# Kernel tuning notes

Measured on AMD Instinct MI355X. Metric: run time of the kernel, lower is better.

Reference implementation:

```python
import jax, jax.numpy as jnp
import numpy as np

N = 30000      # nodes
E = 480000     # edges (before self loops)
DIN = 128      # dim_in
DH = 32        # dim_h (per-head out channels)
H1 = 8         # gat1 heads
H2 = 2         # gat2 heads
G = 64         # num graphs in batch
DOUT = 10      # dim_out
NEG_SLOPE = 0.2


def _glorot(key, shape):
    fan_in = shape[0]
    return jax.random.normal(key, shape, dtype=jnp.float32) / np.sqrt(fan_in)


def setup_inputs() -> dict:
    key = jax.random.key(0)
    ks = jax.random.split(key, 16)
    x = jax.random.normal(ks[0], (N, DIN), dtype=jnp.float32)
    edge_index = jax.random.randint(ks[1], (2, E), 0, N, dtype=jnp.int32)
    batch = jnp.sort(jax.random.randint(ks[2], (N,), 0, G, dtype=jnp.int32))
    # GATv2Conv layer 1: lin_l, lin_r (dim_in -> H1*DH), att (H1, DH), bias (H1*DH)
    W1l = _glorot(ks[3], (DIN, H1 * DH))
    W1r = _glorot(ks[4], (DIN, H1 * DH))
    a1 = _glorot(ks[5], (DH, H1)).T  # [H1, DH]
    b1 = jnp.zeros((H1 * DH,), dtype=jnp.float32)
    # GATv2Conv layer 2: (H1*DH -> H2*DH)
    W2l = _glorot(ks[6], (H1 * DH, H2 * DH))
    W2r = _glorot(ks[7], (H1 * DH, H2 * DH))
    a2 = _glorot(ks[8], (DH, H2)).T  # [H2, DH]
    b2 = jnp.zeros((H2 * DH,), dtype=jnp.float32)
    # MLP head: fc1(2*DH -> DH), fc2(DH -> DH//2), fc(DH//2 -> DOUT); stored [in,out]
    fc1_w = _glorot(ks[9], (2 * DH, DH)); fc1_b = jnp.zeros((DH,), jnp.float32)
    fc2_w = _glorot(ks[10], (DH, DH // 2)); fc2_b = jnp.zeros((DH // 2,), jnp.float32)
    fc_w = _glorot(ks[11], (DH // 2, DOUT)); fc_b = jnp.zeros((DOUT,), jnp.float32)
    return {"x": x, "edge_index": edge_index, "batch": batch,
            "W1l": W1l, "W1r": W1r, "a1": a1, "b1": b1,
            "W2l": W2l, "W2r": W2r, "a2": a2, "b2": b2,
            "fc1_w": fc1_w, "fc1_b": fc1_b, "fc2_w": fc2_w, "fc2_b": fc2_b,
            "fc_w": fc_w, "fc_b": fc_b}


def gatv2_conv(x, edge_index, Wl, Wr, att, bias, heads, dh, n):
    """PyG GATv2Conv: concat=True, add_self_loops=True, negative_slope=0.2."""
    src, dst = edge_index[0], edge_index[1]
    loop = jnp.arange(n, dtype=src.dtype)        # self loops (PyG default)
    src = jnp.concatenate([src, loop])
    dst = jnp.concatenate([dst, loop])
    xl = (x @ Wl).reshape(n, heads, dh)          # source transform
    xr = (x @ Wr).reshape(n, heads, dh)          # destination transform
    xj = xl[src]                                  # [Etot, H, dh] message features
    s = jax.nn.leaky_relu(xj + xr[dst], NEG_SLOPE)
    e = jnp.einsum('ehd,hd->eh', s, att)          # per-edge per-head score
    # segment softmax over incoming edges of each destination node
    m = jax.ops.segment_max(e, dst, num_segments=n)
    p = jnp.exp(e - m[dst])
    z = jax.ops.segment_sum(p, dst, num_segments=n)
    alpha = p / z[dst]                            # [Etot, H]
    out = jax.ops.segment_sum(xj * alpha[..., None], dst, num_segments=n)
    return out.reshape(n, heads * dh) + bias


def reference(x, edge_index, batch, W1l, W1r, a1, b1, W2l, W2r, a2, b2,
              fc1_w, fc1_b, fc2_w, fc2_b, fc_w, fc_b):
    h = gatv2_conv(x, edge_index, W1l, W1r, a1, b1, H1, DH, N)
    h = jax.nn.elu(h)
    h = gatv2_conv(h, edge_index, W2l, W2r, a2, b2, H2, DH, N)  # [N, 2*DH]
    # global_mean_pool
    sums = jax.ops.segment_sum(h, batch, num_segments=G)
    cnt = jax.ops.segment_sum(jnp.ones((N,), h.dtype), batch, num_segments=G)
    hg = sums / jnp.maximum(cnt, 1.0)[:, None]    # [G, 2*DH]
    x1 = jax.nn.relu(hg @ fc1_w + fc1_b)
    # dropout p=0.2 is identity in eval mode
    x2 = jax.nn.relu(x1 @ fc2_w + fc2_b)
    c = x2 @ fc_w + fc_b
    return (c, x2)
```

## Files before the change

### kernel.cpp

```cpp
#include <hip/hip_runtime.h>
#include <math.h>

#define DIN 128
#define DH  32
#define H1  8
#define H2  2
#define GNUM 64
#define DOUT 10
#define NEG_SLOPE 0.2f
#define SCAN_B 512

typedef __attribute__((ext_vector_type(8))) short sv8;
typedef __attribute__((ext_vector_type(4))) short sv4;
typedef __attribute__((ext_vector_type(4))) float fv4;

static __device__ __forceinline__ unsigned short f2bf(float f) {
    unsigned int u = __float_as_uint(f);
    unsigned int r = (u + 0x7fffu + ((u >> 16) & 1u)) >> 16;
    return (unsigned short)r;
}
static __device__ __forceinline__ float bf2f(unsigned short h) {
    return __uint_as_float(((unsigned int)h) << 16);
}

__global__ void k_prep(const float* __restrict__ W1l, const float* __restrict__ W1r,
                       const float* __restrict__ W2l, const float* __restrict__ W2r,
                       short* __restrict__ B1th, short* __restrict__ B1tl,
                       short* __restrict__ B2th, short* __restrict__ B2tl,
                       int* __restrict__ zbase, int nz) {
    int id = blockIdx.x * blockDim.x + threadIdx.x;
    if (id < nz) zbase[id] = 0;
    const int T1 = 512 * 128;
    const int T2 = 128 * 256;
    if (id < T1) {
        int n = id / 128, k = id - n * 128;
        float v = (n < 256) ? W1l[(size_t)k * 256 + n] : W1r[(size_t)k * 256 + (n - 256)];
        unsigned short h = f2bf(v);
        B1th[id] = (short)h;
        B1tl[id] = (short)f2bf(v - bf2f(h));
    } else if (id < T1 + T2) {
        int id2 = id - T1;
        int n = id2 / 256, k = id2 - n * 256;
        float v = (n < 64) ? W2l[(size_t)k * 64 + n] : W2r[(size_t)k * 64 + (n - 64)];
        unsigned short h = f2bf(v);
        B2th[id2] = (short)h;
        B2tl[id2] = (short)f2bf(v - bf2f(h));
    }
}

__global__ void k_deg(const int* __restrict__ dst, int* __restrict__ deg, int E, int n) {
    int i = blockIdx.x * blockDim.x + threadIdx.x;
    if (i < E) {
        atomicAdd(&deg[dst[i]], 1);
    } else if (i < E + n) {
        atomicAdd(&deg[i - E], 1);
    }
}

__global__ __launch_bounds__(SCAN_B)
void k_scan_partial(const int* __restrict__ deg, int* __restrict__ bsum, int n) {
    int i = blockIdx.x * SCAN_B + threadIdx.x;
    int v = (i < n) ? deg[i] : 0;
    #pragma unroll
    for (int m = 32; m >= 1; m >>= 1) v += __shfl_xor(v, m);
    __shared__ int red[SCAN_B / 64];
    if ((threadIdx.x & 63) == 0) red[threadIdx.x >> 6] = v;
    __syncthreads();
    if (threadIdx.x == 0) {
        int s = 0;
        #pragma unroll
        for (int k = 0; k < SCAN_B / 64; ++k) s += red[k];
        bsum[blockIdx.x] = s;
    }
}

__global__ __launch_bounds__(SCAN_B)
void k_scan_apply(int* __restrict__ deg, int* __restrict__ cursor,
                  const int* __restrict__ bsum, int n, int nb) {
    __shared__ int buf[SCAN_B];
    __shared__ int pfx_s, tot_s;
    const int t = threadIdx.x, b = blockIdx.x;
    if (t < 64) {
        int v = (t < nb) ? bsum[t] : 0;
        int incl = v;
        #pragma unroll
        for (int o = 1; o < 64; o <<= 1) {
            int w = __shfl_up(incl, o);
            if (t >= o) incl += w;
        }
        int pfx = (b == 0) ? 0 : __shfl(incl, b - 1);
        int tot = __shfl(incl, nb - 1);
        if (t == 0) { pfx_s = pfx; tot_s = tot; }
    }
    int i = b * SCAN_B + t;
    int v = (i < n) ? deg[i] : 0;
    buf[t] = v;
    __syncthreads();
    for (int o = 1; o < SCAN_B; o <<= 1) {
        int a = (t >= o) ? buf[t - o] : 0;
        __syncthreads();
        buf[t] += a;
        __syncthreads();
    }
    int excl = buf[t] - v + pfx_s;
    if (i < n) { deg[i] = excl; cursor[i] = excl; }
    if (b == 0 && t == 0) deg[n] = tot_s;
}

__global__ void k_scatter(const int* __restrict__ src, const int* __restrict__ dst,
                          int* __restrict__ cursor, int* __restrict__ csr_src, int E, int n) {
    int i = blockIdx.x * blockDim.x + threadIdx.x;
    if (i < E) {
        int d = dst[i];
        int pos = atomicAdd(&cursor[d], 1);
        csr_src[pos] = src[i];
    } else if (i < E + n) {
        int v = i - E;
        int pos = atomicAdd(&cursor[v], 1);
        csr_src[pos] = v;
    }
}

__global__ __launch_bounds__(256)
void k_gemm1(const float* __restrict__ A,
             const short* __restrict__ Bth, const short* __restrict__ Btl,
             unsigned short* __restrict__ C,
             int M, int K, int Ntot) {
    __shared__ union {
        struct { short hi[128 * 40]; short lo[128 * 40]; } a;
        float c[64 * 68];
    } sm;
    const int tid = threadIdx.x;
    const int lane = tid & 63;
    const int wid = tid >> 6;
    const int wm = wid & 1, wn = wid >> 1;
    const int m0 = blockIdx.x * 128;
    const int n0 = blockIdx.y * 128;
    const int l15 = lane & 15, q = lane >> 4;

    fv4 acc[4][4] = {};

    for (int kk = 0; kk < K; kk += 32) {
        __syncthreads();
        #pragma unroll
        for (int i = 0; i < 4; ++i) {
            int idx = tid + i * 256;
            int row = idx >> 3;
            int qq  = idx & 7;
            int mg  = m0 + row;
            float4 v = make_float4(0.f, 0.f, 0.f, 0.f);
            if (mg < M) v = *(const float4*)(A + (size_t)mg * K + kk + qq * 4);
            unsigned short hx = f2bf(v.x), hy = f2bf(v.y), hz = f2bf(v.z), hw = f2bf(v.w);
            sv4 hi = { (short)hx, (short)hy, (short)hz, (short)hw };
            sv4 lo = { (short)f2bf(v.x - bf2f(hx)), (short)f2bf(v.y - bf2f(hy)),
                       (short)f2bf(v.z - bf2f(hz)), (short)f2bf(v.w - bf2f(hw)) };
            *(sv4*)&sm.a.hi[row * 40 + qq * 4] = hi;
            *(sv4*)&sm.a.lo[row * 40 + qq * 4] = lo;
        }
        __syncthreads();

        sv8 bh[4], bl[4];
        #pragma unroll
        for (int fn = 0; fn < 4; ++fn) {
            int ng = n0 + wn * 64 + fn * 16 + l15;
            bh[fn] = *(const sv8*)(Bth + (size_t)ng * K + kk + q * 8);
            bl[fn] = *(const sv8*)(Btl + (size_t)ng * K + kk + q * 8);
        }
        #pragma unroll
        for (int fm = 0; fm < 4; ++fm) {
            int rl = wm * 64 + fm * 16 + l15;
            sv8 ah = *(const sv8*)&sm.a.hi[rl * 40 + q * 8];
            sv8 al = *(const sv8*)&sm.a.lo[rl * 40 + q * 8];
            #pragma unroll
            for (int fn = 0; fn < 4; ++fn) {
                acc[fm][fn] = __builtin_amdgcn_mfma_f32_16x16x32_bf16(ah, bh[fn], acc[fm][fn], 0, 0, 0);
                acc[fm][fn] = __builtin_amdgcn_mfma_f32_16x16x32_bf16(ah, bl[fn], acc[fm][fn], 0, 0, 0);
                acc[fm][fn] = __builtin_amdgcn_mfma_f32_16x16x32_bf16(al, bh[fn], acc[fm][fn], 0, 0, 0);
            }
        }
    }

    #pragma unroll
    for (int s = 0; s < 2; ++s) {
        #pragma unroll
        for (int cn = 0; cn < 2; ++cn) {
            __syncthreads();
            if (wm == s && wn == cn) {
                #pragma unroll
                for (int fm = 0; fm < 4; ++fm)
                    #pragma unroll
                    for (int fn = 0; fn < 4; ++fn)
                        #pragma unroll
                        for (int r = 0; r < 4; ++r)
                            sm.c[(fm * 16 + q * 4 + r) * 68 + fn * 16 + l15] = acc[fm][fn][r];
            }
            __syncthreads();
            int lr = tid >> 2;
            int grow = m0 + s * 64 + lr;
            if (grow < M) {
                #pragma unroll
                for (int k4 = 0; k4 < 4; ++k4) {
                    int jj = (tid & 3) + k4 * 4;
                    float4 vv = *(float4*)&sm.c[lr * 68 + jj * 4];
                    int gcol = n0 + cn * 64 + jj * 4;
                    ushort4 uu;
                    uu.x = f2bf(vv.x); uu.y = f2bf(vv.y);
                    uu.z = f2bf(vv.z); uu.w = f2bf(vv.w);
                    *(ushort4*)(C + (size_t)grow * Ntot + gcol) = uu;
                }
            }
        }
    }
}

__global__ __launch_bounds__(256)
void k_gemm_bf(const unsigned short* __restrict__ A, const short* __restrict__ Bth,
               const short* __restrict__ Btl,
               unsigned short* __restrict__ C,
               int M, int K, int Ntot) {
    __shared__ union {
        short a[128 * 40];
        float c[64 * 68];
    } sm;
    const int tid = threadIdx.x;
    const int lane = tid & 63;
    const int wid = tid >> 6;
    const int wm = wid & 1, wn = wid >> 1;
    const int m0 = blockIdx.x * 128;
    const int n0 = blockIdx.y * 128;
    const int l15 = lane & 15, q = lane >> 4;

    fv4 acc[4][4] = {};

    for (int kk = 0; kk < K; kk += 32) {
        __syncthreads();
        #pragma unroll
        for (int i = 0; i < 2; ++i) {
            int idx = tid + i * 256;
            int row = idx >> 2, qq = idx & 3;
            int mg = m0 + row;
            sv8 v = { 0, 0, 0, 0, 0, 0, 0, 0 };
            if (mg < M) v = *(const sv8*)(A + (size_t)mg * K + kk + qq * 8);
            *(sv8*)&sm.a[row * 40 + qq * 8] = v;
        }
        __syncthreads();

        sv8 bh[4], bl[4];
        #pragma unroll
        for (int fn = 0; fn < 4; ++fn) {
            int ng = n0 + wn * 64 + fn * 16 + l15;
            bh[fn] = *(const sv8*)(Bth + (size_t)ng * K + kk + q * 8);
            bl[fn] = *(const sv8*)(Btl + (size_t)ng * K + kk + q * 8);
        }
        #pragma unroll
        for (int fm = 0; fm < 4; ++fm) {
            int rl = wm * 64 + fm * 16 + l15;
            sv8 ah = *(const sv8*)&sm.a[rl * 40 + q * 8];
            #pragma unroll
            for (int fn = 0; fn < 4; ++fn) {
                acc[fm][fn] = __builtin_amdgcn_mfma_f32_16x16x32_bf16(ah, bh[fn], acc[fm][fn], 0, 0, 0);
                acc[fm][fn] = __builtin_amdgcn_mfma_f32_16x16x32_bf16(ah, bl[fn], acc[fm][fn], 0, 0, 0);
            }
        }
    }

    #pragma unroll
    for (int s = 0; s < 2; ++s) {
        #pragma unroll
        for (int cn = 0; cn < 2; ++cn) {
            __syncthreads();
            if (wm == s && wn == cn) {
                #pragma unroll
                for (int fm = 0; fm < 4; ++fm)
                    #pragma unroll
                    for (int fn = 0; fn < 4; ++fn)
                        #pragma unroll
                        for (int r = 0; r < 4; ++r)
                            sm.c[(fm * 16 + q * 4 + r) * 68 + fn * 16 + l15] = acc[fm][fn][r];
            }
            __syncthreads();
            int lr = tid >> 2;
            int grow = m0 + s * 64 + lr;
            if (grow < M) {
                #pragma unroll
                for (int k4 = 0; k4 < 4; ++k4) {
                    int jj = (tid & 3) + k4 * 4;
                    float4 vv = *(float4*)&sm.c[lr * 68 + jj * 4];
                    int gcol = n0 + cn * 64 + jj * 4;
                    ushort4 uu;
                    uu.x = f2bf(vv.x); uu.y = f2bf(vv.y);
                    uu.z = f2bf(vv.z); uu.w = f2bf(vv.w);
                    *(ushort4*)(C + (size_t)grow * Ntot + gcol) = uu;
                }
            }
        }
    }
}

__global__ __launch_bounds__(64)
void k_edge1(const unsigned short* __restrict__ XLR,
             const int* __restrict__ offs, const int* __restrict__ csr,
             const float* __restrict__ att, const float* __restrict__ bias,
             unsigned short* __restrict__ out, int n) {
    const int lane = threadIdx.x;
    const int v = blockIdx.x;
    const int li = lane & 31;
    const int half = lane >> 5;
    const uint4* XL4 = (const uint4*)XLR;
    float av[8], xr[8];
    #pragma unroll
    for (int k = 0; k < 8; ++k) av[k] = att[li * 8 + k];
    {
        uint4 u = XL4[(size_t)v * 64 + 32 + li];
        xr[0] = __uint_as_float(u.x << 16);  xr[1] = __uint_as_float(u.x & 0xffff0000u);
        xr[2] = __uint_as_float(u.y << 16);  xr[3] = __uint_as_float(u.y & 0xffff0000u);
        xr[4] = __uint_as_float(u.z << 16);  xr[5] = __uint_as_float(u.z & 0xffff0000u);
        xr[6] = __uint_as_float(u.w << 16);  xr[7] = __uint_as_float(u.w & 0xffff0000u);
    }
    float z = 0.f;
    float acc[8] = {};
    const int e0 = offs[v], e1 = offs[v + 1];
    for (int j0 = e0; j0 < e1; j0 += 4) {
        #pragma unroll
        for (int p = 0; p < 2; ++p) {
            int j = j0 + p * 2 + half;
            bool valid = (j < e1);
            int jj = valid ? j : (e1 - 1);
            int src = csr[jj];
            uint4 u = XL4[(size_t)src * 64 + li];
            float f[8];
            f[0] = __uint_as_float(u.x << 16);  f[1] = __uint_as_float(u.x & 0xffff0000u);
            f[2] = __uint_as_float(u.y << 16);  f[3] = __uint_as_float(u.y & 0xffff0000u);
            f[4] = __uint_as_float(u.z << 16);  f[5] = __uint_as_float(u.z & 0xffff0000u);
            f[6] = __uint_as_float(u.w << 16);  f[7] = __uint_as_float(u.w & 0xffff0000u);
            float s1 = 0.f, s2 = 0.f;
            #pragma unroll
            for (int k = 0; k < 8; ++k) {
                float t = f[k] + xr[k];
                s1 = fmaf(t, av[k], s1);
                s2 = fmaf(fabsf(t), av[k], s2);
            }
            float s = fmaf(0.6f, s1, 0.4f * s2);
            s += __shfl_xor(s, 1);
            s += __shfl_xor(s, 2);
            float w = valid ? __expf(s) : 0.f;
            z += w;
            #pragma unroll
            for (int k = 0; k < 8; ++k) acc[k] = fmaf(w, f[k], acc[k]);
        }
    }
    z += __shfl_xor(z, 32);
    #pragma unroll
    for (int k = 0; k < 8; ++k) acc[k] += __shfl_xor(acc[k], 32);
    if (half == 0) {
        const float rz = 1.f / z;
        unsigned int o[4];
        #pragma unroll
        for (int k2 = 0; k2 < 4; ++k2) {
            float lo = fmaf(acc[k2 * 2 + 0], rz, bias[li * 8 + k2 * 2 + 0]);
            float hi = fmaf(acc[k2 * 2 + 1], rz, bias[li * 8 + k2 * 2 + 1]);
            lo = (lo > 0.f) ? lo : (__expf(lo) - 1.f);
            hi = (hi > 0.f) ? hi : (__expf(hi) - 1.f);
            o[k2] = (unsigned int)f2bf(lo) | ((unsigned int)f2bf(hi) << 16);
        }
        uint4 ov = { o[0], o[1], o[2], o[3] };
        *(uint4*)(out + (size_t)v * 256 + li * 8) = ov;
    }
}

__global__ __launch_bounds__(64)
void k_edge2(const unsigned short* __restrict__ XLR,
             const int* __restrict__ offs, const int* __restrict__ csr,
             const float* __restrict__ att, const float* __restrict__ bias,
             float* __restrict__ out, int n) {
    const int lane = threadIdx.x;
    const int v = blockIdx.x;
    const int li = lane & 7;
    const int slot = lane >> 3;
    const uint4* XL4 = (const uint4*)XLR;
    float av[8], xr[8];
    #pragma unroll
    for (int k = 0; k < 8; ++k) av[k] = att[li * 8 + k];
    {
        uint4 u = XL4[(size_t)v * 16 + 8 + li];
        xr[0] = __uint_as_float(u.x << 16);  xr[1] = __uint_as_float(u.x & 0xffff0000u);
        xr[2] = __uint_as_float(u.y << 16);  xr[3] = __uint_as_float(u.y & 0xffff0000u);
        xr[4] = __uint_as_float(u.z << 16);  xr[5] = __uint_as_float(u.z & 0xffff0000u);
        xr[6] = __uint_as_float(u.w << 16);  xr[7] = __uint_as_float(u.w & 0xffff0000u);
    }
    float z = 0.f;
    float acc[8] = {};
    const int e0 = offs[v], e1 = offs[v + 1];
    for (int j0 = e0; j0 < e1; j0 += 8) {
        int j = j0 + slot;
        bool valid = (j < e1);
        int jj = valid ? j : (e1 - 1);
        int src = csr[jj];
        uint4 u = XL4[(size_t)src * 16 + li];
        float f[8];
        f[0] = __uint_as_float(u.x << 16);  f[1] = __uint_as_float(u.x & 0xffff0000u);
        f[2] = __uint_as_float(u.y << 16);  f[3] = __uint_as_float(u.y & 0xffff0000u);
        f[4] = __uint_as_float(u.z << 16);  f[5] = __uint_as_float(u.z & 0xffff0000u);
        f[6] = __uint_as_float(u.w << 16);  f[7] = __uint_as_float(u.w & 0xffff0000u);
        float s1 = 0.f, s2 = 0.f;
        #pragma unroll
        for (int k = 0; k < 8; ++k) {
            float t = f[k] + xr[k];
            s1 = fmaf(t, av[k], s1);
            s2 = fmaf(fabsf(t), av[k], s2);
        }
        float s = fmaf(0.6f, s1, 0.4f * s2);
        s += __shfl_xor(s, 1);
        s += __shfl_xor(s, 2);
        float w = valid ? __expf(s) : 0.f;
        z += w;
        #pragma unroll
        for (int k = 0; k < 8; ++k) acc[k] = fmaf(w, f[k], acc[k]);
    }
    z += __shfl_xor(z, 8);  z += __shfl_xor(z, 16);  z += __shfl_xor(z, 32);
    #pragma unroll
    for (int k = 0; k < 8; ++k) {
        acc[k] += __shfl_xor(acc[k], 8);
        acc[k] += __shfl_xor(acc[k], 16);
        acc[k] += __shfl_xor(acc[k], 32);
    }
    if (slot == 0) {
        const float rz = 1.f / z;
        float o[8];
        #pragma unroll
        for (int k = 0; k < 8; ++k)
            o[k] = fmaf(acc[k], rz, bias[li * 8 + k]);
        float4 o0 = { o[0], o[1], o[2], o[3] };
        float4 o1 = { o[4], o[5], o[6], o[7] };
        *(float4*)(out + (size_t)v * 64 + li * 8 + 0) = o0;
        *(float4*)(out + (size_t)v * 64 + li * 8 + 4) = o1;
    }
}

__global__ __launch_bounds__(256)
void k_pool_mlp(const float* __restrict__ out2, const int* __restrict__ batch,
                const float* __restrict__ fc1w, const float* __restrict__ fc1b,
                const float* __restrict__ fc2w, const float* __restrict__ fc2b,
                const float* __restrict__ fcw,  const float* __restrict__ fcb,
                float* __restrict__ outc, float* __restrict__ outx2, int n) {
    const int g = blockIdx.x;
    const int t = threadIdx.x;
    const int lane = t & 63;
    const int w = t >> 6;
    __shared__ float red[4][64];
    __shared__ float hg_s[64];
    __shared__ float x1_s[32];
    __shared__ float x2_s[16];

    int lo = 0, hi = n;
    while (lo < hi) { int mid = (lo + hi) >> 1; if (batch[mid] < g) lo = mid + 1; else hi = mid; }
    const int start = lo;
    hi = n;
    while (lo < hi) { int mid = (lo + hi) >> 1; if (batch[mid] < g + 1) lo = mid + 1; else hi = mid; }
    const int end = lo;

    float s = 0.f;
    for (int v = start + w; v < end; v += 4)
        s += out2[(size_t)v * 64 + lane];
    red[w][lane] = s;
    __syncthreads();
    if (w == 0) {
        float tot = red[0][lane] + red[1][lane] + red[2][lane] + red[3][lane];
        float cnt = fmaxf((float)(end - start), 1.0f);
        hg_s[lane] = tot / cnt;
    }
    __syncthreads();
    if (t < 32) {
        float a = fc1b[t];
        #pragma unroll
        for (int k = 0; k < 64; ++k) a = fmaf(hg_s[k], fc1w[k * 32 + t], a);
        x1_s[t] = fmaxf(a, 0.f);
    }
    __syncthreads();
    if (t < 16) {
        float a = fc2b[t];
        #pragma unroll
        for (int k = 0; k < 32; ++k) a = fmaf(x1_s[k], fc2w[k * 16 + t], a);
        x2_s[t] = fmaxf(a, 0.f);
    }
    __syncthreads();
    if (t < DOUT) {
        float a = fcb[t];
        #pragma unroll
        for (int k = 0; k < 16; ++k) a = fmaf(x2_s[k], fcw[k * 10 + t], a);
        outc[g * DOUT + t] = a;
    }
    if (t < 16) outx2[g * 16 + t] = x2_s[t];
}

extern "C" void kernel_launch(void* const* d_in, const int* in_sizes, int n_in,
                              void* d_out, int out_size, void* d_ws, size_t ws_size,
                              hipStream_t stream) {
    const float* x    = (const float*)d_in[0];
    const int*   ei   = (const int*)d_in[1];
    const int*   batch= (const int*)d_in[2];
    const float* W1l  = (const float*)d_in[3];
    const float* W1r  = (const float*)d_in[4];
    const float* a1   = (const float*)d_in[5];
    const float* b1   = (const float*)d_in[6];
    const float* W2l  = (const float*)d_in[7];
    const float* W2r  = (const float*)d_in[8];
    const float* a2   = (const float*)d_in[9];
    const float* b2   = (const float*)d_in[10];
    const float* fc1w = (const float*)d_in[11];
    const float* fc1b = (const float*)d_in[12];
    const float* fc2w = (const float*)d_in[13];
    const float* fc2b = (const float*)d_in[14];
    const float* fcw  = (const float*)d_in[15];
    const float* fcb  = (const float*)d_in[16];

    const int N = in_sizes[2];
    const int E = in_sizes[1] / 2;
    const int ET = E + N;
    const int* esrc = ei;
    const int* edst = ei + E;
    const int NB = (N + SCAN_B - 1) / SCAN_B;

    char* ws = (char*)d_ws;
    size_t off = 0;
    unsigned short* xlr1b = (unsigned short*)(ws + off); off += (size_t)N * 512 * 2;
    unsigned short* h1b  = (unsigned short*)(ws + off);  off += (size_t)N * 256 * 2;
    float* out2 = (float*)(ws + off);            off += (size_t)N * 64 * 4;
    int*   deg   = (int*)(ws + off);             off += ((size_t)(N + 1) * 4 + 255) & ~255ull;
    int*   cursor= (int*)(ws + off);             off += ((size_t)N * 4 + 255) & ~255ull;
    int*   csr   = (int*)(ws + off);             off += ((size_t)ET * 4 + 255) & ~255ull;
    int*   bsum  = (int*)(ws + off);             off += ((size_t)(NB + 1) * 4 + 255) & ~255ull;
    short* B1th  = (short*)(ws + off);           off += (size_t)512 * 128 * 2;
    short* B1tl  = (short*)(ws + off);           off += (size_t)512 * 128 * 2;
    short* B2th  = (short*)(ws + off);           off += (size_t)128 * 256 * 2;
    short* B2tl  = (short*)(ws + off);           off += (size_t)128 * 256 * 2;
    unsigned short* xlr2b = xlr1b;
    (void)ws_size; (void)n_in; (void)out_size;

    float* outc  = (float*)d_out;
    float* outx2 = (float*)d_out + GNUM * DOUT;

    const int prep_tot = 512 * 128 + 128 * 256;
    k_prep<<<(prep_tot + 255) / 256, 256, 0, stream>>>(
        W1l, W1r, W2l, W2r, B1th, B1tl, B2th, B2tl, deg, N + 1);

    int tb = 256;
    int gb = (ET + tb - 1) / tb;
    k_deg<<<gb, tb, 0, stream>>>(edst, deg, E, N);
    k_scan_partial<<<NB, SCAN_B, 0, stream>>>(deg, bsum, N);
    k_scan_apply<<<NB, SCAN_B, 0, stream>>>(deg, cursor, bsum, N, NB);
    k_scatter<<<gb, tb, 0, stream>>>(esrc, edst, cursor, csr, E, N);

    dim3 g1((N + 127) / 128, 4);
    k_gemm1<<<g1, 256, 0, stream>>>(x, B1th, B1tl, xlr1b, N, DIN, 512);

    k_edge1<<<N, 64, 0, stream>>>(xlr1b, deg, csr, a1, b1, h1b, N);

    dim3 g2((N + 127) / 128, 1);
    k_gemm_bf<<<g2, 256, 0, stream>>>(h1b, B2th, B2tl, xlr2b, N, 256, 128);

    k_edge2<<<N, 64, 0, stream>>>(xlr2b, deg, csr, a2, b2, out2, N);

    k_pool_mlp<<<GNUM, 256, 0, stream>>>(out2, batch, fc1w, fc1b, fc2w, fc2b,
                                         fcw, fcb, outc, outx2, N);
}
```

Baseline: 293.0 us.

## Pre-split x into bf16 hi/lo once and load GEMM operands directly from global

The fp32 input x is now converted to packed bf16 hi/lo rows in the prep kernel, so gemm1 no longer redoes the split for every column block. Both GEMMs drop the shared-memory A staging and its per-iteration barriers, loading MFMA fragments straight from global memory and relying on cache. gemm_bf is split into two column blocks of 64 for more parallelism, and launch bounds request two blocks per CU. In exchange there is an extra global buffer of N x 256 bf16 written and read, and the direct global fragment loads are less coalesced.

```diff
diff --git a/kernel.cpp b/kernel.cpp
--- a/kernel.cpp
+++ b/kernel.cpp
@@ -23,25 +23,39 @@
     return __uint_as_float(((unsigned int)h) << 16);
 }
 
-__global__ void k_prep(const float* __restrict__ W1l, const float* __restrict__ W1r,
+__global__ void k_prep(const float* __restrict__ x,
+                       const float* __restrict__ W1l, const float* __restrict__ W1r,
                        const float* __restrict__ W2l, const float* __restrict__ W2r,
+                       unsigned short* __restrict__ xg,
                        short* __restrict__ B1th, short* __restrict__ B1tl,
                        short* __restrict__ B2th, short* __restrict__ B2tl,
-                       int* __restrict__ zbase, int nz) {
+                       int* __restrict__ zbase, int nz, int n) {
     int id = blockIdx.x * blockDim.x + threadIdx.x;
     if (id < nz) zbase[id] = 0;
+    const int NX = n * 32;
     const int T1 = 512 * 128;
     const int T2 = 128 * 256;
-    if (id < T1) {
-        int n = id / 128, k = id - n * 128;
-        float v = (n < 256) ? W1l[(size_t)k * 256 + n] : W1r[(size_t)k * 256 + (n - 256)];
+    if (id < NX) {
+        int m = id >> 5, j = id & 31;
+        float4 v = *(const float4*)(x + (size_t)m * 128 + j * 4);
+        unsigned short hx = f2bf(v.x), hy = f2bf(v.y), hz = f2bf(v.z), hw = f2bf(v.w);
+        ushort4 hi; hi.x = hx; hi.y = hy; hi.z = hz; hi.w = hw;
+        ushort4 lo;
+        lo.x = f2bf(v.x - bf2f(hx)); lo.y = f2bf(v.y - bf2f(hy));
+        lo.z = f2bf(v.z - bf2f(hz)); lo.w = f2bf(v.w - bf2f(hw));
+        *(ushort4*)(xg + (size_t)m * 256 + j * 4) = hi;
+        *(ushort4*)(xg + (size_t)m * 256 + 128 + j * 4) = lo;
+    } else if (id < NX + T1) {
+        int id1 = id - NX;
+        int nn = id1 / 128, k = id1 - nn * 128;
+        float v = (nn < 256) ? W1l[(size_t)k * 256 + nn] : W1r[(size_t)k * 256 + (nn - 256)];
         unsigned short h = f2bf(v);
-        B1th[id] = (short)h;
-        B1tl[id] = (short)f2bf(v - bf2f(h));
-    } else if (id < T1 + T2) {
-        int id2 = id - T1;
-        int n = id2 / 256, k = id2 - n * 256;
-        float v = (n < 64) ? W2l[(size_t)k * 64 + n] : W2r[(size_t)k * 64 + (n - 64)];
+        B1th[id1] = (short)h;
+        B1tl[id1] = (short)f2bf(v - bf2f(h));
+    } else if (id < NX + T1 + T2) {
+        int id2 = id - NX - T1;
+        int nn = id2 / 256, k = id2 - nn * 256;
+        float v = (nn < 64) ? W2l[(size_t)k * 64 + nn] : W2r[(size_t)k * 64 + (nn - 64)];
         unsigned short h = f2bf(v);
         B2th[id2] = (short)h;
         B2tl[id2] = (short)f2bf(v - bf2f(h));
@@ -121,15 +135,12 @@
     }
 }
 
-__global__ __launch_bounds__(256)
-void k_gemm1(const float* __restrict__ A,
+__global__ __launch_bounds__(256, 2)
+void k_gemm1(const unsigned short* __restrict__ Ag,
              const short* __restrict__ Bth, const short* __restrict__ Btl,
              unsigned short* __restrict__ C,
-             int M, int K, int Ntot) {
-    __shared__ union {
-        struct { short hi[128 * 40]; short lo[128 * 40]; } a;
-        float c[64 * 68];
-    } sm;
+             int M, int Ntot) {
+    __shared__ float smc[64 * 68];
     const int tid = threadIdx.x;
     const int lane = tid & 63;
     const int wid = tid >> 6;
@@ -140,42 +151,43 @@
 
     fv4 acc[4][4] = {};
 
-    for (int kk = 0; kk < K; kk += 32) {
-        __syncthreads();
-        #pragma unroll
-        for (int i = 0; i < 4; ++i) {
-            int idx = tid + i * 256;
-            int row = idx >> 3;
-            int qq  = idx & 7;
-            int mg  = m0 + row;
-            float4 v = make_float4(0.f, 0.f, 0.f, 0.f);
-            if (mg < M) v = *(const float4*)(A + (size_t)mg * K + kk + qq * 4);
-            unsigned short hx = f2bf(v.x), hy = f2bf(v.y), hz = f2bf(v.z), hw = f2bf(v.w);
-            sv4 hi = { (short)hx, (short)hy, (short)hz, (short)hw };
-            sv4 lo = { (short)f2bf(v.x - bf2f(hx)), (short)f2bf(v.y - bf2f(hy)),
-                       (short)f2bf(v.z - bf2f(hz)), (short)f2bf(v.w - bf2f(hw)) };
-            *(sv4*)&sm.a.hi[row * 40 + qq * 4] = hi;
-            *(sv4*)&sm.a.lo[row * 40 + qq * 4] = lo;
-        }
-        __syncthreads();
-
-        sv8 bh[4], bl[4];
+    const unsigned short* arow[4];
+    #pragma unroll
+    for (int fm = 0; fm < 4; ++fm) {
+        int mg = m0 + wm * 64 + fm * 16 + l15;
+        if (mg >= M) mg = M - 1;
+        arow[fm] = Ag + (size_t)mg * 256;
+    }
+    const short* browh[4];
+    const short* browl[4];
+    #pragma unroll
+    for (int fn = 0; fn < 4; ++fn) {
+        int ng = n0 + wn * 64 + fn * 16 + l15;
+        browh[fn] = Bth + (size_t)ng * 128;
+        browl[fn] = Btl + (size_t)ng * 128;
+    }
+
+    #pragma unroll
+    for (int c = 0; c < 4; ++c) {
+        const int ko = c * 32 + q * 8;
+        sv8 ah[4], al[4], bh[4], bl[4];
         #pragma unroll
         for (int fn = 0; fn < 4; ++fn) {
-            int ng = n0 + wn * 64 + fn * 16 + l15;
-            bh[fn] = *(const sv8*)(Bth + (size_t)ng * K + kk + q * 8);
-            bl[fn] = *(const sv8*)(Btl + (size_t)ng * K + kk + q * 8);
+            bh[fn] = *(const sv8*)(browh[fn] + ko);
+            bl[fn] = *(const sv8*)(browl[fn] + ko);
         }
         #pragma unroll
         for (int fm = 0; fm < 4; ++fm) {
-            int rl = wm * 64 + fm * 16 + l15;
-            sv8 ah = *(const sv8*)&sm.a.hi[rl * 40 + q * 8];
-            sv8 al = *(const sv8*)&sm.a.lo[rl * 40 + q * 8];
+            ah[fm] = *(const sv8*)(arow[fm] + ko);
+            al[fm] = *(const sv8*)(arow[fm] + 128 + ko);
+        }
+        #pragma unroll
+        for (int fm = 0; fm < 4; ++fm) {
             #pragma unroll
             for (int fn = 0; fn < 4; ++fn) {
-                acc[fm][fn] = __builtin_amdgcn_mfma_f32_16x16x32_bf16(ah, bh[fn], acc[fm][fn], 0, 0, 0);
-                acc[fm][fn] = __builtin_amdgcn_mfma_f32_16x16x32_bf16(ah, bl[fn], acc[fm][fn], 0, 0, 0);
-                acc[fm][fn] = __builtin_amdgcn_mfma_f32_16x16x32_bf16(al, bh[fn], acc[fm][fn], 0, 0, 0);
+                acc[fm][fn] = __builtin_amdgcn_mfma_f32_16x16x32_bf16(ah[fm], bh[fn], acc[fm][fn], 0, 0, 0);
+                acc[fm][fn] = __builtin_amdgcn_mfma_f32_16x16x32_bf16(ah[fm], bl[fn], acc[fm][fn], 0, 0, 0);
+                acc[fm][fn] = __builtin_amdgcn_mfma_f32_16x16x32_bf16(al[fm], bh[fn], acc[fm][fn], 0, 0, 0);
             }
         }
     }
@@ -192,7 +204,7 @@
                     for (int fn = 0; fn < 4; ++fn)
                         #pragma unroll
                         for (int r = 0; r < 4; ++r)
-                            sm.c[(fm * 16 + q * 4 + r) * 68 + fn * 16 + l15] = acc[fm][fn][r];
+                            smc[(fm * 16 + q * 4 + r) * 68 + fn * 16 + l15] = acc[fm][fn][r];
             }
             __syncthreads();
             int lr = tid >> 2;
@@ -201,7 +213,7 @@
                 #pragma unroll
                 for (int k4 = 0; k4 < 4; ++k4) {
                     int jj = (tid & 3) + k4 * 4;
-                    float4 vv = *(float4*)&sm.c[lr * 68 + jj * 4];
+                    float4 vv = *(float4*)&smc[lr * 68 + jj * 4];
                     int gcol = n0 + cn * 64 + jj * 4;
                     ushort4 uu;
                     uu.x = f2bf(vv.x); uu.y = f2bf(vv.y);
@@ -213,53 +225,56 @@
     }
 }
 
-__global__ __launch_bounds__(256)
+__global__ __launch_bounds__(256, 2)
 void k_gemm_bf(const unsigned short* __restrict__ A, const short* __restrict__ Bth,
                const short* __restrict__ Btl,
                unsigned short* __restrict__ C,
-               int M, int K, int Ntot) {
-    __shared__ union {
-        short a[128 * 40];
-        float c[64 * 68];
-    } sm;
+               int M, int Ntot) {
+    __shared__ float smc[64 * 36];
     const int tid = threadIdx.x;
     const int lane = tid & 63;
     const int wid = tid >> 6;
     const int wm = wid & 1, wn = wid >> 1;
     const int m0 = blockIdx.x * 128;
-    const int n0 = blockIdx.y * 128;
+    const int n0 = blockIdx.y * 64;
     const int l15 = lane & 15, q = lane >> 4;
 
-    fv4 acc[4][4] = {};
-
-    for (int kk = 0; kk < K; kk += 32) {
-        __syncthreads();
-        #pragma unroll
-        for (int i = 0; i < 2; ++i) {
-            int idx = tid + i * 256;
-            int row = idx >> 2, qq = idx & 3;
-            int mg = m0 + row;
-            sv8 v = { 0, 0, 0, 0, 0, 0, 0, 0 };
-            if (mg < M) v = *(const sv8*)(A + (size_t)mg * K + kk + qq * 8);
-            *(sv8*)&sm.a[row * 40 + qq * 8] = v;
-        }
-        __syncthreads();
-
-        sv8 bh[4], bl[4];
-        #pragma unroll
-        for (int fn = 0; fn < 4; ++fn) {
-            int ng = n0 + wn * 64 + fn * 16 + l15;
-            bh[fn] = *(const sv8*)(Bth + (size_t)ng * K + kk + q * 8);
-            bl[fn] = *(const sv8*)(Btl + (size_t)ng * K + kk + q * 8);
-        }
+    fv4 acc[4][2] = {};
+
+    const unsigned short* arow[4];
+    #pragma unroll
+    for (int fm = 0; fm < 4; ++fm) {
+        int mg = m0 + wm * 64 + fm * 16 + l15;
+        if (mg >= M) mg = M - 1;
+        arow[fm] = A + (size_t)mg * 256;
+    }
+    const short* browh[2];
+    const short* browl[2];
+    #pragma unroll
+    for (int fn = 0; fn < 2; ++fn) {
+        int ng = n0 + wn * 32 + fn * 16 + l15;
+        browh[fn] = Bth + (size_t)ng * 256;
+        browl[fn] = Btl + (size_t)ng * 256;
+    }
+
+    #pragma unroll 4
+    for (int c = 0; c < 8; ++c) {
+        const int ko = c * 32 + q * 8;
+        sv8 ah[4], bh[2], bl[2];
+        #pragma unroll
+        for (int fn = 0; fn < 2; ++fn) {
+            bh[fn] = *(const sv8*)(browh[fn] + ko);
+            bl[fn] = *(const sv8*)(browl[fn] + ko);
+        }
+        #pragma unroll
+        for (int fm = 0; fm < 4; ++fm)
+            ah[fm] = *(const sv8*)(arow[fm] + ko);
         #pragma unroll
         for (int fm = 0; fm < 4; ++fm) {
-            int rl = wm * 64 + fm * 16 + l15;
-            sv8 ah = *(const sv8*)&sm.a[rl * 40 + q * 8];
             #pragma unroll
-            for (int fn = 0; fn < 4; ++fn) {
-                acc[fm][fn] = __builtin_amdgcn_mfma_f32_16x16x32_bf16(ah, bh[fn], acc[fm][fn], 0, 0, 0);
-                acc[fm][fn] = __builtin_amdgcn_mfma_f32_16x16x32_bf16(ah, bl[fn], acc[fm][fn], 0, 0, 0);
+            for (int fn = 0; fn < 2; ++fn) {
+                acc[fm][fn] = __builtin_amdgcn_mfma_f32_16x16x32_bf16(ah[fm], bh[fn], acc[fm][fn], 0, 0, 0);
+                acc[fm][fn] = __builtin_amdgcn_mfma_f32_16x16x32_bf16(ah[fm], bl[fn], acc[fm][fn], 0, 0, 0);
             }
         }
     }
@@ -273,20 +288,20 @@
                 #pragma unroll
                 for (int fm = 0; fm < 4; ++fm)
                     #pragma unroll
-                    for (int fn = 0; fn < 4; ++fn)
+                    for (int fn = 0; fn < 2; ++fn)
                         #pragma unroll
                         for (int r = 0; r < 4; ++r)
-                            sm.c[(fm * 16 + q * 4 + r) * 68 + fn * 16 + l15] = acc[fm][fn][r];
+                            smc[(fm * 16 + q * 4 + r) * 36 + fn * 16 + l15] = acc[fm][fn][r];
             }
             __syncthreads();
             int lr = tid >> 2;
             int grow = m0 + s * 64 + lr;
             if (grow < M) {
                 #pragma unroll
-                for (int k4 = 0; k4 < 4; ++k4) {
+                for (int k4 = 0; k4 < 2; ++k4) {
                     int jj = (tid & 3) + k4 * 4;
-                    float4 vv = *(float4*)&sm.c[lr * 68 + jj * 4];
-                    int gcol = n0 + cn * 64 + jj * 4;
+                    float4 vv = *(float4*)&smc[lr * 36 + jj * 4];
+                    int gcol = n0 + cn * 32 + jj * 4;
                     ushort4 uu;
                     uu.x = f2bf(vv.x); uu.y = f2bf(vv.y);
                     uu.z = f2bf(vv.z); uu.w = f2bf(vv.w);
@@ -534,15 +549,16 @@
     short* B1tl  = (short*)(ws + off);           off += (size_t)512 * 128 * 2;
     short* B2th  = (short*)(ws + off);           off += (size_t)128 * 256 * 2;
     short* B2tl  = (short*)(ws + off);           off += (size_t)128 * 256 * 2;
+    unsigned short* xg = (unsigned short*)(ws + off); off += (size_t)N * 256 * 2;
     unsigned short* xlr2b = xlr1b;
     (void)ws_size; (void)n_in; (void)out_size;
 
     float* outc  = (float*)d_out;
     float* outx2 = (float*)d_out + GNUM * DOUT;
 
-    const int prep_tot = 512 * 128 + 128 * 256;
+    const int prep_tot = N * 32 + 512 * 128 + 128 * 256;
     k_prep<<<(prep_tot + 255) / 256, 256, 0, stream>>>(
-        W1l, W1r, W2l, W2r, B1th, B1tl, B2th, B2tl, deg, N + 1);
+        x, W1l, W1r, W2l, W2r, xg, B1th, B1tl, B2th, B2tl, deg, N + 1, N);
 
     int tb = 256;
     int gb = (ET + tb - 1) / tb;
@@ -552,12 +568,12 @@
     k_scatter<<<gb, tb, 0, stream>>>(esrc, edst, cursor, csr, E, N);
 
     dim3 g1((N + 127) / 128, 4);
-    k_gemm1<<<g1, 256, 0, stream>>>(x, B1th, B1tl, xlr1b, N, DIN, 512);
+    k_gemm1<<<g1, 256, 0, stream>>>(xg, B1th, B1tl, xlr1b, N, 512);
 
     k_edge1<<<N, 64, 0, stream>>>(xlr1b, deg, csr, a1, b1, h1b, N);
 
-    dim3 g2((N + 127) / 128, 1);
-    k_gemm_bf<<<g2, 256, 0, stream>>>(h1b, B2th, B2tl, xlr2b, N, 256, 128);
+    dim3 g2((N + 127) / 128, 2);
+    k_gemm_bf<<<g2, 256, 0, stream>>>(h1b, B2th, B2tl, xlr2b, N, 128);
 
     k_edge2<<<N, 64, 0, stream>>>(xlr2b, deg, csr, a2, b2, out2, N);
 
```

Result: no change. 295.8 us (+1.0%).
